# Kernel tuning notes

Measured on AMD Instinct MI355X. Metric: run time of the kernel, lower is better.

The kernel has to match this reference:

```python
import jax, jax.numpy as jnp
import numpy as np

N = 50000      # nodes
E = 800000     # edges (before self loops)
IN_DIM = 256
HID = 64       # per-head hidden dim
HEADS = 4
NEG_SLOPE = 0.2


def setup_inputs() -> dict:
    key = jax.random.key(0)
    k1, k2, k3, k4, k5, k6 = jax.random.split(key, 6)
    x = jax.random.normal(k1, (N, IN_DIM), dtype=jnp.float32)
    edge_index = jax.random.randint(k2, (2, E), 0, N, dtype=jnp.int64)
    # GATConv params (PyG layout): lin weight, att_src, att_dst, bias
    W = jax.random.normal(k3, (IN_DIM, HEADS * HID), dtype=jnp.float32) / np.sqrt(IN_DIM)
    att_src = jax.random.normal(k4, (HEADS, HID), dtype=jnp.float32) / np.sqrt(HID)
    att_dst = jax.random.normal(k5, (HEADS, HID), dtype=jnp.float32) / np.sqrt(HID)
    bias = jnp.zeros((HEADS * HID,), dtype=jnp.float32)
    return {"x": x, "edge_index": edge_index, "W": W,
            "att_src": att_src, "att_dst": att_dst, "bias": bias}


def _gat_forward(x, edge_index, W, att_src, att_dst, bias):
    n = x.shape[0]
    # linear projection per head: [N, H, F]
    h = (x @ W).reshape(n, HEADS, HID)
    # per-node attention logits (computed once on nodes, then gathered)
    a_src = jnp.einsum('nhf,hf->nh', h, att_src)  # [N, H]
    a_dst = jnp.einsum('nhf,hf->nh', h, att_dst)  # [N, H]
    # add self loops (PyG default add_self_loops=True)
    loop = jnp.arange(n, dtype=edge_index.dtype)
    src = jnp.concatenate([edge_index[0], loop])  # [E+N]
    dst = jnp.concatenate([edge_index[1], loop])  # [E+N]
    # edge attention logits with LeakyReLU
    e = jax.nn.leaky_relu(a_src[src] + a_dst[dst], NEG_SLOPE)  # [E+N, H]
    # segment softmax over incoming edges of each destination node
    m = jax.ops.segment_max(e, dst, num_segments=n)            # [N, H]
    num = jnp.exp(e - m[dst])                                  # [E+N, H]
    denom = jax.ops.segment_sum(num, dst, num_segments=n)      # [N, H]
    alpha = num / denom[dst]                                   # [E+N, H]
    # scatter-aggregate weighted source features
    msg = alpha[:, :, None] * h[src]                           # [E+N, H, F]
    out = jax.ops.segment_sum(msg, dst, num_segments=n)        # [N, H, F]
    out = out.reshape(n, HEADS * HID) + bias
    # GraphEncoder.forward: ReLU then Dropout (dropout=0 -> identity)
    return jax.nn.relu(out)


def reference(x, edge_index, W, att_src, att_dst, bias):
    return _gat_forward(x, edge_index, W, att_src, att_dst, bias)
```

## Files before the change

### kernel.cpp

```cpp
#include <hip/hip_runtime.h>
#include <hip/hip_bf16.h>

#define N_NODES 50000
#define N_EDGES 800000
#define TOT_EDGES (N_EDGES + N_NODES)
#define IN_DIM 256
#define OUT_DIM 256
#define HEADS 4
#define NEG_SLOPE 0.2f
#define CAP 96

#define FBLK 256
#define NGB  768
#define NT   1563
#define LDS_STRIDE 264

typedef __bf16 bf16x8 __attribute__((ext_vector_type(8)));
typedef __bf16 bf16x4 __attribute__((ext_vector_type(4)));
typedef float f32x4 __attribute__((ext_vector_type(4)));

__device__ __forceinline__ float b2f(unsigned short u) {
    union { float f; unsigned int i; } v; v.i = ((unsigned int)u) << 16; return v.f;
}

struct Args {
    const float* x; const int* ei; const float* W;
    const float* att_s; const float* att_d; const float* bias;
    float* out;
    __bf16* Wt; __bf16* h; float* a_src; float* a_dst;
    int* counts; int* ell;
};

__global__ void k_wt(Args A) {
    int k = blockIdx.x;
    int n = threadIdx.x;
    A.Wt[(size_t)n * IN_DIM + k] = (__bf16)A.W[(size_t)k * OUT_DIM + n];
    int idx = blockIdx.x * 256 + threadIdx.x;
    if (idx < N_NODES) A.counts[idx] = 0;
}

__global__ __launch_bounds__(512, 4) void k_gemm_fill(Args A) {
    __shared__ __bf16 xs[32 * LDS_STRIDE];
    __shared__ __bf16 tr[32 * LDS_STRIDE];
    __shared__ float  lg[2][8][32];
    const int t = threadIdx.x;

    if (blockIdx.x >= FBLK) {
        const int g    = blockIdx.x - FBLK;
        const int wave = t >> 6;
        const int lane = t & 63;
        const int cc   = lane & 15;
        const int quad = lane >> 4;
        const int n0   = wave * 32;

        bf16x8 Bf[8][2];
#pragma unroll
        for (int kk = 0; kk < 8; ++kk)
#pragma unroll
            for (int f = 0; f < 2; ++f)
                Bf[kk][f] = *(const bf16x8*)(A.Wt
                    + (size_t)(n0 + f * 16 + cc) * IN_DIM + kk * 32 + quad * 8);
        float as0 = A.att_s[n0 + cc], as1 = A.att_s[n0 + 16 + cc];
        float ad0 = A.att_d[n0 + cc], ad1 = A.att_d[n0 + 16 + cc];

        const float4* x4 = (const float4*)A.x;

        float4 st[4];
#pragma unroll
        for (int i = 0; i < 4; ++i) {
            int f = i * 512 + t;
            int row = f >> 6, c4 = f & 63;
            int grow = g * 32 + row; if (grow >= N_NODES) grow = N_NODES - 1;
            st[i] = x4[(size_t)grow * 64 + c4];
        }
#pragma unroll
        for (int i = 0; i < 4; ++i) {
            int f = i * 512 + t;
            int row = f >> 6, c4 = f & 63;
            bf16x4 o = { (__bf16)st[i].x, (__bf16)st[i].y, (__bf16)st[i].z, (__bf16)st[i].w };
            *(bf16x4*)&xs[row * LDS_STRIDE + c4 * 4] = o;
        }
        __syncthreads();

        for (int tile = g; tile < NT; tile += NGB) {
            const int next = tile + NGB;
            const bool hn = next < NT;
            float4 st2[4];
            if (hn) {
#pragma unroll
                for (int i = 0; i < 4; ++i) {
                    int f = i * 512 + t;
                    int row = f >> 6, c4 = f & 63;
                    int grow = next * 32 + row; if (grow >= N_NODES) grow = N_NODES - 1;
                    st2[i] = x4[(size_t)grow * 64 + c4];
                }
            }

            f32x4 acc[2][2];
#pragma unroll
            for (int mt = 0; mt < 2; ++mt)
#pragma unroll
                for (int f = 0; f < 2; ++f) acc[mt][f] = (f32x4){0.f, 0.f, 0.f, 0.f};
#pragma unroll
            for (int kk = 0; kk < 8; ++kk) {
#pragma unroll
                for (int mt = 0; mt < 2; ++mt) {
                    bf16x8 a = *(const bf16x8*)&xs[(mt * 16 + cc) * LDS_STRIDE + kk * 32 + quad * 8];
                    acc[mt][0] = __builtin_amdgcn_mfma_f32_16x16x32_bf16(a, Bf[kk][0], acc[mt][0], 0, 0, 0);
                    acc[mt][1] = __builtin_amdgcn_mfma_f32_16x16x32_bf16(a, Bf[kk][1], acc[mt][1], 0, 0, 0);
                }
            }

#pragma unroll
            for (int mt = 0; mt < 2; ++mt) {
#pragma unroll
                for (int r = 0; r < 4; ++r) {
                    float pS = acc[mt][0][r] * as0 + acc[mt][1][r] * as1;
                    float pD = acc[mt][0][r] * ad0 + acc[mt][1][r] * ad1;
#pragma unroll
                    for (int o = 8; o >= 1; o >>= 1) {
                        pS += __shfl_xor(pS, o, 64);
                        pD += __shfl_xor(pD, o, 64);
                    }
                    if (cc == 0) {
                        lg[0][wave][mt * 16 + quad * 4 + r] = pS;
                        lg[1][wave][mt * 16 + quad * 4 + r] = pD;
                    }
                }
            }
            __syncthreads();

            if (hn) {
#pragma unroll
                for (int i = 0; i < 4; ++i) {
                    int f = i * 512 + t;
                    int row = f >> 6, c4 = f & 63;
                    bf16x4 o = { (__bf16)st2[i].x, (__bf16)st2[i].y, (__bf16)st2[i].z, (__bf16)st2[i].w };
                    *(bf16x4*)&xs[row * LDS_STRIDE + c4 * 4] = o;
                }
            }
#pragma unroll
            for (int mt = 0; mt < 2; ++mt)
#pragma unroll
                for (int f = 0; f < 2; ++f)
#pragma unroll
                    for (int r = 0; r < 4; ++r)
                        tr[(mt * 16 + quad * 4 + r) * LDS_STRIDE + n0 + f * 16 + cc] =
                            (__bf16)acc[mt][f][r];
            if (t < 256) {
                int td = t & 127;
                int row = td >> 2, head = td & 3;
                int grow = tile * 32 + row;
                if (grow < N_NODES) {
                    int sd = t >> 7;
                    float v = lg[sd][2 * head][row] + lg[sd][2 * head + 1][row];
                    float* dst = sd == 0 ? A.a_src : A.a_dst;
                    dst[grow * 4 + head] = v;
                }
            }
            __syncthreads();

#pragma unroll
            for (int i = 0; i < 2; ++i) {
                int idx = i * 512 + t;
                int row = idx >> 5, c8 = idx & 31;
                int grow = tile * 32 + row;
                if (grow < N_NODES)
                    *(bf16x8*)(A.h + (size_t)grow * OUT_DIM + c8 * 8) =
                        *(const bf16x8*)&tr[row * LDS_STRIDE + c8 * 8];
            }
        }
    } else {
        int nz = 0;
        for (int i = t; i < 1024; i += 512)
            if (A.ei[2 * i + 1] != 0) nz++;
        bool is64 = (__syncthreads_count(nz) == 0);
        const long long* ei64 = (const long long*)A.ei;
        for (int i = blockIdx.x * 512 + t; i < TOT_EDGES; i += FBLK * 512) {
            int s, d;
            if (i < N_EDGES) {
                if (is64) { s = (int)ei64[i]; d = (int)ei64[N_EDGES + i]; }
                else      { s = A.ei[i];      d = A.ei[N_EDGES + i]; }
            } else {
                s = d = i - N_EDGES;
            }
            int pos = atomicAdd(&A.counts[d], 1);
            if (pos < CAP) A.ell[(size_t)d * CAP + pos] = s;
        }
    }
}

__global__ __launch_bounds__(256) void k_agg(Args A) {
    __shared__ float lds_all[4][CAP][4];
    int wave = threadIdx.x >> 6, lane = threadIdx.x & 63;
    int node = blockIdx.x * 4 + wave;
    if (node >= N_NODES) return;
    float (*lds)[4] = lds_all[wave];

    int base = node * CAP;
    int deg  = A.counts[node];
    if (deg > CAP) deg = CAP;
    const float4* as4 = (const float4*)A.a_src;
    float4 ad = ((const float4*)A.a_dst)[node];

    float4 smv = {0.f, 0.f, 0.f, 0.f};
    for (int e = lane; e < deg; e += 64) {
        int s = A.ell[base + e];
        float4 av = as4[s];
        float4 l;
        l.x = av.x + ad.x; l.x = l.x > 0.f ? l.x : NEG_SLOPE * l.x;
        l.y = av.y + ad.y; l.y = l.y > 0.f ? l.y : NEG_SLOPE * l.y;
        l.z = av.z + ad.z; l.z = l.z > 0.f ? l.z : NEG_SLOPE * l.z;
        l.w = av.w + ad.w; l.w = l.w > 0.f ? l.w : NEG_SLOPE * l.w;
        float4 e4;
        e4.x = __expf(l.x); e4.y = __expf(l.y);
        e4.z = __expf(l.z); e4.w = __expf(l.w);
        smv.x += e4.x; smv.y += e4.y; smv.z += e4.z; smv.w += e4.w;
        lds[e][0] = e4.x; lds[e][1] = e4.y; lds[e][2] = e4.z; lds[e][3] = e4.w;
    }
    int padEnd = (deg + 3) & ~3;
    for (int e = deg + lane; e < padEnd; e += 64) {
        lds[e][0] = 0.f; lds[e][1] = 0.f; lds[e][2] = 0.f; lds[e][3] = 0.f;
    }
#pragma unroll
    for (int o = 32; o >= 1; o >>= 1) {
        smv.x += __shfl_xor(smv.x, o, 64);
        smv.y += __shfl_xor(smv.y, o, 64);
        smv.z += __shfl_xor(smv.z, o, 64);
        smv.w += __shfl_xor(smv.w, o, 64);
    }

    int head = lane >> 4;
    float smh = head == 0 ? smv.x : head == 1 ? smv.y : head == 2 ? smv.z : smv.w;
    float inv_d = 1.f / smh;

    float acc0 = 0.f, acc1 = 0.f, acc2 = 0.f, acc3 = 0.f;
    const unsigned short* hs = reinterpret_cast<const unsigned short*>(A.h);
    int rEnd = padEnd;
    for (int e = 0; e < rEnd; e += 4) {
        int s0 = A.ell[base + e];
        int s1 = A.ell[base + ((e + 1 < deg) ? e + 1 : 0)];
        int s2 = A.ell[base + ((e + 2 < deg) ? e + 2 : 0)];
        int s3 = A.ell[base + ((e + 3 < deg) ? e + 3 : 0)];
        float al0 = lds[e][head];
        float al1 = lds[e + 1][head];
        float al2 = lds[e + 2][head];
        float al3 = lds[e + 3][head];
        ushort4 h0 = *(const ushort4*)(hs + (size_t)s0 * OUT_DIM + lane * 4);
        ushort4 h1 = *(const ushort4*)(hs + (size_t)s1 * OUT_DIM + lane * 4);
        ushort4 h2 = *(const ushort4*)(hs + (size_t)s2 * OUT_DIM + lane * 4);
        ushort4 h3 = *(const ushort4*)(hs + (size_t)s3 * OUT_DIM + lane * 4);
        acc0 += al0 * b2f(h0.x) + al1 * b2f(h1.x) + al2 * b2f(h2.x) + al3 * b2f(h3.x);
        acc1 += al0 * b2f(h0.y) + al1 * b2f(h1.y) + al2 * b2f(h2.y) + al3 * b2f(h3.y);
        acc2 += al0 * b2f(h0.z) + al1 * b2f(h1.z) + al2 * b2f(h2.z) + al3 * b2f(h3.z);
        acc3 += al0 * b2f(h0.w) + al1 * b2f(h1.w) + al2 * b2f(h2.w) + al3 * b2f(h3.w);
    }

    float4 bv = ((const float4*)A.bias)[lane];
    float v0 = acc0 * inv_d + bv.x;
    float v1 = acc1 * inv_d + bv.y;
    float v2 = acc2 * inv_d + bv.z;
    float v3 = acc3 * inv_d + bv.w;
    float4 o4;
    o4.x = v0 > 0.f ? v0 : 0.f;
    o4.y = v1 > 0.f ? v1 : 0.f;
    o4.z = v2 > 0.f ? v2 : 0.f;
    o4.w = v3 > 0.f ? v3 : 0.f;
    ((float4*)A.out)[(size_t)node * 64 + lane] = o4;
}

extern "C" void kernel_launch(void* const* d_in, const int* in_sizes, int n_in,
                              void* d_out, int out_size, void* d_ws, size_t ws_size,
                              hipStream_t stream) {
    (void)out_size; (void)ws_size;
    const void* p_x = nullptr; const void* p_ei = nullptr; const void* p_W = nullptr;
    const void* p_small[3] = {nullptr, nullptr, nullptr}; int nsmall = 0;
    for (int i = 0; i < n_in; ++i) {
        switch (in_sizes[i]) {
            case N_NODES * IN_DIM:      p_x = d_in[i]; break;
            case 2 * N_EDGES:           p_ei = d_in[i]; break;
            case IN_DIM * OUT_DIM:      p_W = d_in[i]; break;
            case OUT_DIM:               if (nsmall < 3) p_small[nsmall++] = d_in[i]; break;
            default: break;
        }
    }
    if (!p_x)  p_x  = d_in[0];
    if (!p_ei) p_ei = d_in[1];
    if (!p_W)  p_W  = d_in[2];
    if (nsmall < 3) { p_small[0] = d_in[3]; p_small[1] = d_in[4]; p_small[2] = d_in[5]; }

    char* ws = (char*)d_ws;
    size_t off = 0;
    auto alloc = [&](size_t bytes) -> void* {
        void* p = ws + off;
        off = (off + bytes + 255) & ~(size_t)255;
        return p;
    };
    Args A;
    A.Wt      = (__bf16*)alloc((size_t)IN_DIM * OUT_DIM * 2);
    A.h       = (__bf16*)alloc((size_t)N_NODES * OUT_DIM * 2);
    A.a_src   = (float*)alloc((size_t)N_NODES * HEADS * 4);
    A.a_dst   = (float*)alloc((size_t)N_NODES * HEADS * 4);
    A.counts  = (int*)alloc((size_t)N_NODES * 4);
    A.ell     = (int*)alloc((size_t)N_NODES * CAP * 4);

    A.x     = (const float*)p_x;
    A.ei    = (const int*)p_ei;
    A.W     = (const float*)p_W;
    A.att_s = (const float*)p_small[0];
    A.att_d = (const float*)p_small[1];
    A.bias  = (const float*)p_small[2];
    A.out   = (float*)d_out;

    k_wt<<<dim3(IN_DIM), dim3(OUT_DIM), 0, stream>>>(A);
    k_gemm_fill<<<dim3(FBLK + NGB), dim3(512), 0, stream>>>(A);
    k_agg<<<dim3((N_NODES + 3) / 4), dim3(256), 0, stream>>>(A);
}
```

Baseline: 246.1 us.

## Launch one GEMM block per tile and drop software prefetch loop

Replaces the persistent grid-stride GEMM loop (768 blocks, each prefetching its next x tile into registers) with one block per 32-row tile (1563 blocks). The separate transpose LDS buffer is dropped by reusing xs for output staging, and the launch-bounds occupancy hint goes from 4 to 2 blocks. The aggregation kernel's output store becomes a nontemporal store. The aim is to rely on more resident blocks for latency hiding instead of explicit prefetch, at the cost of reloading W fragments into registers in every block.

Result: no change. 241.7 us (-1.8%).

```diff
diff --git a/kernel.cpp b/kernel.cpp
--- a/kernel.cpp
+++ b/kernel.cpp
@@ -11,7 +11,6 @@
 #define CAP 96
 
 #define FBLK 256
-#define NGB  768
 #define NT   1563
 #define LDS_STRIDE 264
 
@@ -39,38 +38,37 @@
     if (idx < N_NODES) A.counts[idx] = 0;
 }
 
-__global__ __launch_bounds__(512, 4) void k_gemm_fill(Args A) {
+__global__ __launch_bounds__(512, 2) void k_gemm_fill(Args A) {
     __shared__ __bf16 xs[32 * LDS_STRIDE];
-    __shared__ __bf16 tr[32 * LDS_STRIDE];
     __shared__ float  lg[2][8][32];
     const int t = threadIdx.x;
 
     if (blockIdx.x >= FBLK) {
-        const int g    = blockIdx.x - FBLK;
+        const int tile = blockIdx.x - FBLK;
         const int wave = t >> 6;
         const int lane = t & 63;
         const int cc   = lane & 15;
         const int quad = lane >> 4;
         const int n0   = wave * 32;
+        const __bf16* __restrict__ Wt = A.Wt;
+        const float4* __restrict__ x4 = (const float4*)A.x;
 
         bf16x8 Bf[8][2];
 #pragma unroll
         for (int kk = 0; kk < 8; ++kk)
 #pragma unroll
             for (int f = 0; f < 2; ++f)
-                Bf[kk][f] = *(const bf16x8*)(A.Wt
+                Bf[kk][f] = *(const bf16x8*)(Wt
                     + (size_t)(n0 + f * 16 + cc) * IN_DIM + kk * 32 + quad * 8);
         float as0 = A.att_s[n0 + cc], as1 = A.att_s[n0 + 16 + cc];
         float ad0 = A.att_d[n0 + cc], ad1 = A.att_d[n0 + 16 + cc];
 
-        const float4* x4 = (const float4*)A.x;
-
         float4 st[4];
 #pragma unroll
         for (int i = 0; i < 4; ++i) {
             int f = i * 512 + t;
             int row = f >> 6, c4 = f & 63;
-            int grow = g * 32 + row; if (grow >= N_NODES) grow = N_NODES - 1;
+            int grow = tile * 32 + row; if (grow >= N_NODES) grow = N_NODES - 1;
             st[i] = x4[(size_t)grow * 64 + c4];
         }
 #pragma unroll
@@ -82,93 +80,69 @@
         }
         __syncthreads();
 
-        for (int tile = g; tile < NT; tile += NGB) {
-            const int next = tile + NGB;
-            const bool hn = next < NT;
-            float4 st2[4];
-            if (hn) {
-#pragma unroll
-                for (int i = 0; i < 4; ++i) {
-                    int f = i * 512 + t;
-                    int row = f >> 6, c4 = f & 63;
-                    int grow = next * 32 + row; if (grow >= N_NODES) grow = N_NODES - 1;
-                    st2[i] = x4[(size_t)grow * 64 + c4];
+        f32x4 acc[2][2];
+#pragma unroll
+        for (int mt = 0; mt < 2; ++mt)
+#pragma unroll
+            for (int f = 0; f < 2; ++f) acc[mt][f] = (f32x4){0.f, 0.f, 0.f, 0.f};
+#pragma unroll
+        for (int kk = 0; kk < 8; ++kk) {
+#pragma unroll
+            for (int mt = 0; mt < 2; ++mt) {
+                bf16x8 a = *(const bf16x8*)&xs[(mt * 16 + cc) * LDS_STRIDE + kk * 32 + quad * 8];
+                acc[mt][0] = __builtin_amdgcn_mfma_f32_16x16x32_bf16(a, Bf[kk][0], acc[mt][0], 0, 0, 0);
+                acc[mt][1] = __builtin_amdgcn_mfma_f32_16x16x32_bf16(a, Bf[kk][1], acc[mt][1], 0, 0, 0);
+            }
+        }
+
+#pragma unroll
+        for (int mt = 0; mt < 2; ++mt) {
+#pragma unroll
+            for (int r = 0; r < 4; ++r) {
+                float pS = acc[mt][0][r] * as0 + acc[mt][1][r] * as1;
+                float pD = acc[mt][0][r] * ad0 + acc[mt][1][r] * ad1;
+#pragma unroll
+                for (int o = 8; o >= 1; o >>= 1) {
+                    pS += __shfl_xor(pS, o, 64);
+                    pD += __shfl_xor(pD, o, 64);
                 }
-            }
-
-            f32x4 acc[2][2];
-#pragma unroll
-            for (int mt = 0; mt < 2; ++mt)
-#pragma unroll
-                for (int f = 0; f < 2; ++f) acc[mt][f] = (f32x4){0.f, 0.f, 0.f, 0.f};
-#pragma unroll
-            for (int kk = 0; kk < 8; ++kk) {
-#pragma unroll
-                for (int mt = 0; mt < 2; ++mt) {
-                    bf16x8 a = *(const bf16x8*)&xs[(mt * 16 + cc) * LDS_STRIDE + kk * 32 + quad * 8];
-                    acc[mt][0] = __builtin_amdgcn_mfma_f32_16x16x32_bf16(a, Bf[kk][0], acc[mt][0], 0, 0, 0);
-                    acc[mt][1] = __builtin_amdgcn_mfma_f32_16x16x32_bf16(a, Bf[kk][1], acc[mt][1], 0, 0, 0);
+                if (cc == 0) {
+                    lg[0][wave][mt * 16 + quad * 4 + r] = pS;
+                    lg[1][wave][mt * 16 + quad * 4 + r] = pD;
                 }
             }
-
-#pragma unroll
-            for (int mt = 0; mt < 2; ++mt) {
-#pragma unroll
-                for (int r = 0; r < 4; ++r) {
-                    float pS = acc[mt][0][r] * as0 + acc[mt][1][r] * as1;
-                    float pD = acc[mt][0][r] * ad0 + acc[mt][1][r] * ad1;
-#pragma unroll
-                    for (int o = 8; o >= 1; o >>= 1) {
-                        pS += __shfl_xor(pS, o, 64);
-                        pD += __shfl_xor(pD, o, 64);
-                    }
-                    if (cc == 0) {
-                        lg[0][wave][mt * 16 + quad * 4 + r] = pS;
-                        lg[1][wave][mt * 16 + quad * 4 + r] = pD;
-                    }
-                }
-            }
-            __syncthreads();
-
-            if (hn) {
-#pragma unroll
-                for (int i = 0; i < 4; ++i) {
-                    int f = i * 512 + t;
-                    int row = f >> 6, c4 = f & 63;
-                    bf16x4 o = { (__bf16)st2[i].x, (__bf16)st2[i].y, (__bf16)st2[i].z, (__bf16)st2[i].w };
-                    *(bf16x4*)&xs[row * LDS_STRIDE + c4 * 4] = o;
-                }
-            }
-#pragma unroll
-            for (int mt = 0; mt < 2; ++mt)
-#pragma unroll
-                for (int f = 0; f < 2; ++f)
-#pragma unroll
-                    for (int r = 0; r < 4; ++r)
-                        tr[(mt * 16 + quad * 4 + r) * LDS_STRIDE + n0 + f * 16 + cc] =
-                            (__bf16)acc[mt][f][r];
-            if (t < 256) {
-                int td = t & 127;
-                int row = td >> 2, head = td & 3;
-                int grow = tile * 32 + row;
-                if (grow < N_NODES) {
-                    int sd = t >> 7;
-                    float v = lg[sd][2 * head][row] + lg[sd][2 * head + 1][row];
-                    float* dst = sd == 0 ? A.a_src : A.a_dst;
-                    dst[grow * 4 + head] = v;
-                }
-            }
-            __syncthreads();
-
-#pragma unroll
-            for (int i = 0; i < 2; ++i) {
-                int idx = i * 512 + t;
-                int row = idx >> 5, c8 = idx & 31;
-                int grow = tile * 32 + row;
-                if (grow < N_NODES)
-                    *(bf16x8*)(A.h + (size_t)grow * OUT_DIM + c8 * 8) =
-                        *(const bf16x8*)&tr[row * LDS_STRIDE + c8 * 8];
-            }
+        }
+        __syncthreads();
+
+#pragma unroll
+        for (int mt = 0; mt < 2; ++mt)
+#pragma unroll
+            for (int f = 0; f < 2; ++f)
+#pragma unroll
+                for (int r = 0; r < 4; ++r)
+                    xs[(mt * 16 + quad * 4 + r) * LDS_STRIDE + n0 + f * 16 + cc] =
+                        (__bf16)acc[mt][f][r];
+        if (t < 256) {
+            int td = t & 127;
+            int row = td >> 2, head = td & 3;
+            int grow = tile * 32 + row;
+            if (grow < N_NODES) {
+                int sd = t >> 7;
+                float v = lg[sd][2 * head][row] + lg[sd][2 * head + 1][row];
+                float* dst = sd == 0 ? A.a_src : A.a_dst;
+                dst[grow * 4 + head] = v;
+            }
+        }
+        __syncthreads();
+
+#pragma unroll
+        for (int i = 0; i < 2; ++i) {
+            int idx = i * 512 + t;
+            int row = idx >> 5, c8 = idx & 31;
+            int grow = tile * 32 + row;
+            if (grow < N_NODES)
+                *(bf16x8*)(A.h + (size_t)grow * OUT_DIM + c8 * 8) =
+                    *(const bf16x8*)&xs[row * LDS_STRIDE + c8 * 8];
         }
     } else {
         int nz = 0;
@@ -257,16 +231,16 @@
     }
 
     float4 bv = ((const float4*)A.bias)[lane];
+    f32x4 o4;
     float v0 = acc0 * inv_d + bv.x;
     float v1 = acc1 * inv_d + bv.y;
     float v2 = acc2 * inv_d + bv.z;
     float v3 = acc3 * inv_d + bv.w;
-    float4 o4;
-    o4.x = v0 > 0.f ? v0 : 0.f;
-    o4.y = v1 > 0.f ? v1 : 0.f;
-    o4.z = v2 > 0.f ? v2 : 0.f;
-    o4.w = v3 > 0.f ? v3 : 0.f;
-    ((float4*)A.out)[(size_t)node * 64 + lane] = o4;
+    o4[0] = v0 > 0.f ? v0 : 0.f;
+    o4[1] = v1 > 0.f ? v1 : 0.f;
+    o4[2] = v2 > 0.f ? v2 : 0.f;
+    o4[3] = v3 > 0.f ? v3 : 0.f;
+    __builtin_nontemporal_store(o4, (f32x4*)A.out + (size_t)node * 64 + lane);
 }
 
 extern "C" void kernel_launch(void* const* d_in, const int* in_sizes, int n_in,
@@ -313,6 +287,6 @@
     A.out   = (float*)d_out;
 
     k_wt<<<dim3(IN_DIM), dim3(OUT_DIM), 0, stream>>>(A);
-    k_gemm_fill<<<dim3(FBLK + NGB), dim3(512), 0, stream>>>(A);
+    k_gemm_fill<<<dim3(FBLK + NT), dim3(512), 0, stream>>>(A);
     k_agg<<<dim3((N_NODES + 3) / 4), dim3(256), 0, stream>>>(A);
 }
```
